# Performance work log

Hardware: AMD Instinct MI355X
Metric: run time of the kernel (lower is better)

Reference implementation:

```python
import math
import jax, jax.numpy as jnp
import numpy as np

NUM_EXPERTS = 8
TOP_K = 2
HIDDEN = 1024
INTER = 4096
CAPACITY_FACTOR = 1.25
S, B = 2048, 4


def setup_inputs() -> dict:
    key = jax.random.key(0)
    k1, k2, k3, k4 = jax.random.split(key, 4)
    hidden_states = jax.random.normal(k1, (S, B, HIDDEN), dtype=jnp.float32)
    T = S * B
    logits = jax.random.normal(k2, (T, NUM_EXPERTS), dtype=jnp.float32)
    expert_affinities = jax.nn.softmax(logits, axis=-1)  # (T, E), normalized per token
    # top-k chosen experts per token (no duplicates), consistent with affinities
    _, expert_index = jax.lax.top_k(expert_affinities, TOP_K)  # (T, top_k) int32
    gate_up_proj = jax.random.normal(k3, (NUM_EXPERTS, HIDDEN, 2 * INTER), dtype=jnp.float32) * 0.02
    down_proj = jax.random.normal(k4, (NUM_EXPERTS, INTER, HIDDEN), dtype=jnp.float32) * 0.02
    return {
        "hidden_states": hidden_states,
        "expert_affinities": expert_affinities,
        "expert_index": expert_index.astype(jnp.int32),
        "gate_up_proj": gate_up_proj,
        "down_proj": down_proj,
    }


def reference(hidden_states, expert_affinities, expert_index, gate_up_proj, down_proj):
    S_, B_, H = hidden_states.shape
    T = S_ * B_
    E = expert_affinities.shape[1]
    K = expert_index.shape[1]
    # expert capacity (static, as in compute_position_in_expert)
    C = min(math.ceil(T * K * CAPACITY_FACTOR / E), T)

    x = hidden_states.reshape(T, H)

    # top_k-hot expert mask (T, E)
    expert_mask = jnp.sum(jax.nn.one_hot(expert_index, E, dtype=jnp.int32), axis=1)
    # 1-indexed position of each token within each chosen expert
    position_in_expert = jnp.cumsum(expert_mask, axis=0) * expert_mask  # (T, E)
    kept = (expert_mask > 0) & (position_in_expert <= C)  # capacity drop
    pos0 = position_in_expert - 1  # 0-indexed

    # gather per-(token, k) positions / keep flags
    pos_tk = jnp.take_along_axis(pos0, expert_index, axis=1)          # (T, K)
    kept_tk = jnp.take_along_axis(kept, expert_index, axis=1)         # (T, K)
    flat_idx = jnp.where(kept_tk, expert_index * C + pos_tk, E * C)   # dropped -> dummy slot

    # dispatch: scatter tokens into per-expert buffers (E*C [+1 dummy], H)
    src = jnp.broadcast_to(x[:, None, :], (T, K, H)).reshape(T * K, H)
    dispatched = jnp.zeros((E * C + 1, H), dtype=x.dtype).at[flat_idx.reshape(-1)].add(src)
    expert_buf = dispatched[: E * C].reshape(E, C, H)

    # grouped expert MLP (GLU): gate/up projection, SiLU gating, down projection
    gate_up = jnp.einsum("ech,ehf->ecf", expert_buf, gate_up_proj)    # (E, C, 2I)
    gate, up = jnp.split(gate_up, 2, axis=2)
    intermediate = jax.nn.silu(gate) * up                              # (E, C, I)
    expert_out = jnp.einsum("eci,eih->ech", intermediate, down_proj)   # (E, C, H)

    # combine: gather each token's expert outputs, weight by (normalized) affinities
    out_flat = jnp.concatenate(
        [expert_out.reshape(E * C, H), jnp.zeros((1, H), dtype=expert_out.dtype)], axis=0
    )
    aff_tk = jnp.take_along_axis(expert_affinities, expert_index, axis=1)  # (T, K)
    aff_tk = aff_tk / jnp.sum(aff_tk, axis=-1, keepdims=True)  # normalize_top_k_affinities
    weights = aff_tk * kept_tk.astype(aff_tk.dtype)            # dropped tokens contribute 0
    tok_out = jnp.sum(out_flat[flat_idx] * weights[..., None], axis=1)  # (T, H)
    return tok_out.reshape(S_, B_, H)
```

## Files before the change

kernel.cpp:

```cpp
#include <hip/hip_runtime.h>
#include <hip/hip_bf16.h>

#define NE 8
#define HID 1024
#define INT_ 4096
#define NTOK 8192
#define CAP 2560

typedef short short8 __attribute__((ext_vector_type(8)));
typedef float floatx4 __attribute__((ext_vector_type(4)));

__device__ __forceinline__ unsigned short f2bf(float f) {
  union { float f; unsigned int u; } v; v.f = f;
  unsigned int u = v.u;
  return (unsigned short)((u + 0x7fffu + ((u >> 16) & 1u)) >> 16);
}

__device__ __forceinline__ void gl2lds16(const void* g, void* l) {
  __builtin_amdgcn_global_load_lds(
      (const __attribute__((address_space(1))) unsigned int*)g,
      (__attribute__((address_space(3))) unsigned int*)l, 16, 0, 0);
}

__global__ void routing_kernel(const int* __restrict__ eidx,
                               int* __restrict__ tfs,
                               int* __restrict__ counts, int* __restrict__ slots) {
  __shared__ unsigned long long masks[128];
  __shared__ int ccnt[128];
  int e = blockIdx.x;
  int tid = threadIdx.x;
  int wave = tid >> 6, lane = tid & 63;

  for (int ch = wave; ch < 128; ch += 4) {
    int t = ch * 64 + lane;
    int2 pr = ((const int2*)eidx)[t];
    bool chosen = (pr.x == e) || (pr.y == e);
    unsigned long long m = __ballot(chosen);
    if (lane == 0) { masks[ch] = m; ccnt[ch] = __popcll(m); }
  }
  __syncthreads();
  if (tid == 0) {
    int run = 0;
    for (int i = 0; i < 128; ++i) { int c = ccnt[i]; ccnt[i] = run; run += c; }
    counts[e] = run < CAP ? run : CAP;
  }
  __syncthreads();
  for (int ch = wave; ch < 128; ch += 4) {
    int t = ch * 64 + lane;
    unsigned long long m = masks[ch];
    if ((m >> lane) & 1ull) {
      int pos = ccnt[ch] + __popcll(m & ((2ull << lane) - 1ull));
      int2 pr = ((const int2*)eidx)[t];
      int kk = (pr.x == e) ? 0 : 1;
      if (pos <= CAP) {
        int slot = e * CAP + pos - 1;
        tfs[slot] = t;
        slots[2 * t + kk] = slot;
      } else {
        slots[2 * t + kk] = -1;
      }
    }
  }
}

__global__ void transpose_cvt_kernel(const float* __restrict__ in, unsigned short* __restrict__ out,
                                     int R, int Cc) {
  __shared__ unsigned short tile[64 * 66];
  int z = blockIdx.z;
  int r0 = blockIdx.y * 64, c0 = blockIdx.x * 64;
  const float* inp = in + (size_t)z * R * Cc;
  unsigned short* outp = out + (size_t)z * R * Cc;
  int tx = threadIdx.x & 15, ty = threadIdx.x >> 4;
#pragma unroll
  for (int j = 0; j < 4; ++j) {
    int r = ty + j * 16;
    float4 v = *(const float4*)(inp + (size_t)(r0 + r) * Cc + c0 + 4 * tx);
    tile[r * 66 + 4 * tx + 0] = f2bf(v.x);
    tile[r * 66 + 4 * tx + 1] = f2bf(v.y);
    tile[r * 66 + 4 * tx + 2] = f2bf(v.z);
    tile[r * 66 + 4 * tx + 3] = f2bf(v.w);
  }
  __syncthreads();
#pragma unroll
  for (int j = 0; j < 4; ++j) {
    int c = ty + j * 16;
    ushort4 p;
    p.x = tile[(4 * tx + 0) * 66 + c];
    p.y = tile[(4 * tx + 1) * 66 + c];
    p.z = tile[(4 * tx + 2) * 66 + c];
    p.w = tile[(4 * tx + 3) * 66 + c];
    *(ushort4*)(outp + (size_t)(c0 + c) * R + r0 + 4 * tx) = p;
  }
}

__global__ void dispatch_kernel(const float* __restrict__ x, const int* __restrict__ tfs,
                                const int* __restrict__ counts, unsigned short* __restrict__ ebuf) {
  int slot = blockIdx.x;
  int e = slot / CAP, c = slot - e * CAP;
  bool valid = c < counts[e];
  int t = valid ? tfs[slot] : 0;
  const float4* src = (const float4*)(x + (size_t)t * HID);
  ushort4* dst = (ushort4*)(ebuf + (size_t)slot * HID);
#pragma unroll
  for (int j = 0; j < 2; ++j) {
    int i = threadIdx.x + j * 128;
    ushort4 p;
    if (valid) {
      float4 v = src[i];
      p.x = f2bf(v.x); p.y = f2bf(v.y); p.z = f2bf(v.z); p.w = f2bf(v.w);
    } else {
      p.x = p.y = p.z = p.w = 0;
    }
    dst[i] = p;
  }
}

__global__ void gemm1_kernel(const unsigned short* __restrict__ ebuf,
                             const unsigned short* __restrict__ wgu,
                             const int* __restrict__ counts,
                             unsigned short* __restrict__ inter) {
  int e = blockIdx.z;
  int c0 = blockIdx.y * 128;
  int f0 = blockIdx.x * 64;
  int cnt = counts[e];
  if (c0 >= cnt) return;

  __shared__ alignas(16) unsigned short smem[16384];
  unsigned short* sA = smem;
  unsigned short* sBg = smem + 8192;
  unsigned short* sBu = smem + 12288;

  int tid = threadIdx.x;
  int wave = tid >> 6, lane = tid & 63;
  int wm = (wave & 1) * 64;
  int isUp = wave >> 1;
  int lrow = lane >> 3, lch = lane & 7;
  int quad = lane >> 4, rl = lane & 15;

  const unsigned short* Ab = ebuf + ((size_t)e * CAP + c0) * HID;
  const unsigned short* Bb = wgu + ((size_t)e * 2 * INT_ + isUp * INT_ + f0) * HID;
  unsigned short* sB = isUp ? sBu : sBg;

  floatx4 acc[4][4];
#pragma unroll
  for (int i = 0; i < 4; ++i)
#pragma unroll
    for (int j = 0; j < 4; ++j) acc[i][j] = (floatx4){0.f, 0.f, 0.f, 0.f};

  for (int kk = 0; kk < HID; kk += 64) {
    __syncthreads();
#pragma unroll
    for (int i = 0; i < 4; ++i) {
      int r = wave * 32 + i * 8 + lrow;
      int gk = kk + ((lch ^ (r & 7)) << 3);
      gl2lds16(Ab + (size_t)r * HID + gk, sA + (wave * 32 + i * 8) * 64);
    }
#pragma unroll
    for (int i = 0; i < 4; ++i) {
      int r = (wave & 1) * 32 + i * 8 + lrow;
      int gk = kk + ((lch ^ (r & 7)) << 3);
      gl2lds16(Bb + (size_t)r * HID + gk, sB + ((wave & 1) * 32 + i * 8) * 64);
    }
    __syncthreads();
#pragma unroll
    for (int ks = 0; ks < 2; ++ks) {
      short8 a[4], b[4];
#pragma unroll
      for (int mi = 0; mi < 4; ++mi) {
        int r = wm + mi * 16 + rl;
        int pc = (ks * 4 + quad) ^ (r & 7);
        a[mi] = *(const short8*)(sA + r * 64 + pc * 8);
      }
#pragma unroll
      for (int ni = 0; ni < 4; ++ni) {
        int r = ni * 16 + rl;
        int pc = (ks * 4 + quad) ^ (r & 7);
        b[ni] = *(const short8*)(sB + r * 64 + pc * 8);
      }
#pragma unroll
      for (int mi = 0; mi < 4; ++mi)
#pragma unroll
        for (int ni = 0; ni < 4; ++ni)
          acc[mi][ni] = __builtin_amdgcn_mfma_f32_16x16x32_bf16(a[mi], b[ni], acc[mi][ni], 0, 0, 0);
    }
  }

  __syncthreads();
  float* gsh = (float*)smem;
  if (!isUp) {
#pragma unroll
    for (int mi = 0; mi < 4; ++mi)
#pragma unroll
      for (int ni = 0; ni < 4; ++ni)
#pragma unroll
        for (int r = 0; r < 4; ++r) {
          int row = wm + mi * 16 + quad * 4 + r;
          int col = ni * 16 + rl;
          gsh[row * 64 + col] = acc[mi][ni][r];
        }
  }
  __syncthreads();
  if (isUp) {
#pragma unroll
    for (int mi = 0; mi < 4; ++mi) {
#pragma unroll
      for (int r = 0; r < 4; ++r) {
        int row = wm + mi * 16 + quad * 4 + r;
#pragma unroll
        for (int ni = 0; ni < 4; ++ni) {
          int col = ni * 16 + rl;
          float g = gsh[row * 64 + col];
          float u = acc[mi][ni][r];
          float s = g / (1.f + __expf(-g));
          inter[((size_t)e * CAP + c0 + row) * INT_ + f0 + col] = f2bf(s * u);
        }
      }
    }
  }
}

__global__ void gemm2_kernel(const unsigned short* __restrict__ inter,
                             const unsigned short* __restrict__ wd,
                             const int* __restrict__ counts,
                             float* __restrict__ eout) {
  int e = blockIdx.z;
  int c0 = blockIdx.y * 128;
  int h0 = blockIdx.x * 128;
  int cnt = counts[e];
  if (c0 >= cnt) return;

  __shared__ alignas(16) unsigned short smem[16384];
  unsigned short* sA = smem;
  unsigned short* sB = smem + 8192;

  int tid = threadIdx.x;
  int wave = tid >> 6, lane = tid & 63;
  int wm = (wave & 1) * 64, wn = (wave >> 1) * 64;
  int lrow = lane >> 3, lch = lane & 7;
  int quad = lane >> 4, rl = lane & 15;

  const unsigned short* Ab = inter + ((size_t)e * CAP + c0) * INT_;
  const unsigned short* Bb = wd + ((size_t)e * HID + h0) * INT_;

  floatx4 acc[4][4];
#pragma unroll
  for (int i = 0; i < 4; ++i)
#pragma unroll
    for (int j = 0; j < 4; ++j) acc[i][j] = (floatx4){0.f, 0.f, 0.f, 0.f};

  for (int kk = 0; kk < INT_; kk += 64) {
    __syncthreads();
#pragma unroll
    for (int i = 0; i < 4; ++i) {
      int r = wave * 32 + i * 8 + lrow;
      int gk = kk + ((lch ^ (r & 7)) << 3);
      gl2lds16(Ab + (size_t)r * INT_ + gk, sA + (wave * 32 + i * 8) * 64);
      gl2lds16(Bb + (size_t)r * INT_ + gk, sB + (wave * 32 + i * 8) * 64);
    }
    __syncthreads();
#pragma unroll
    for (int ks = 0; ks < 2; ++ks) {
      short8 a[4], b[4];
#pragma unroll
      for (int mi = 0; mi < 4; ++mi) {
        int r = wm + mi * 16 + rl;
        int pc = (ks * 4 + quad) ^ (r & 7);
        a[mi] = *(const short8*)(sA + r * 64 + pc * 8);
      }
#pragma unroll
      for (int ni = 0; ni < 4; ++ni) {
        int r = wn + ni * 16 + rl;
        int pc = (ks * 4 + quad) ^ (r & 7);
        b[ni] = *(const short8*)(sB + r * 64 + pc * 8);
      }
#pragma unroll
      for (int mi = 0; mi < 4; ++mi)
#pragma unroll
        for (int ni = 0; ni < 4; ++ni)
          acc[mi][ni] = __builtin_amdgcn_mfma_f32_16x16x32_bf16(a[mi], b[ni], acc[mi][ni], 0, 0, 0);
    }
  }

#pragma unroll
  for (int mi = 0; mi < 4; ++mi) {
#pragma unroll
    for (int r = 0; r < 4; ++r) {
      int row = wm + mi * 16 + quad * 4 + r;
      float* op = eout + ((size_t)e * CAP + c0 + row) * HID + h0;
#pragma unroll
      for (int ni = 0; ni < 4; ++ni) op[wn + ni * 16 + rl] = acc[mi][ni][r];
    }
  }
}

__global__ void combine_kernel(const float4* __restrict__ eout, const int* __restrict__ slots,
                               const float* __restrict__ aff, const int* __restrict__ eidx,
                               float4* __restrict__ out) {
  int t = blockIdx.x;
  int i = threadIdx.x;
  int s0 = slots[2 * t], s1 = slots[2 * t + 1];
  int e0 = eidx[2 * t], e1 = eidx[2 * t + 1];
  float a0 = aff[t * NE + e0], a1 = aff[t * NE + e1];
  float inv = 1.f / (a0 + a1);
  float w0 = (s0 >= 0) ? a0 * inv : 0.f;
  float w1 = (s1 >= 0) ? a1 * inv : 0.f;
  int p0 = (s0 >= 0) ? s0 : 0;
  int p1 = (s1 >= 0) ? s1 : 0;
  float4 v0 = eout[(size_t)p0 * 256 + i];
  float4 v1 = eout[(size_t)p1 * 256 + i];
  float4 r;
  r.x = w0 * v0.x + w1 * v1.x;
  r.y = w0 * v0.y + w1 * v1.y;
  r.z = w0 * v0.z + w1 * v1.z;
  r.w = w0 * v0.w + w1 * v1.w;
  out[(size_t)t * 256 + i] = r;
}

extern "C" void kernel_launch(void* const* d_in, const int* in_sizes, int n_in,
                              void* d_out, int out_size, void* d_ws, size_t ws_size,
                              hipStream_t stream) {
  const float* x = (const float*)d_in[0];
  const float* aff = (const float*)d_in[1];
  const int* eidx = (const int*)d_in[2];
  const float* wgu_f = (const float*)d_in[3];
  const float* wd_f = (const float*)d_in[4];
  float* out = (float*)d_out;

  char* ws = (char*)d_ws;
  int* tfs = (int*)(ws + 0);
  int* counts = (int*)(ws + 163840);
  int* slots = (int*)(ws + 196608);
  unsigned short* ebuf = (unsigned short*)(ws + 262144);
  unsigned short* wgu = (unsigned short*)(ws + 42205184);
  unsigned short* wd = (unsigned short*)(ws + 176422912);
  unsigned short* inter = (unsigned short*)(ws + 243531776);
  float* eout = (float*)(ws + 42205184);

  routing_kernel<<<NE, 256, 0, stream>>>(eidx, tfs, counts, slots);
  transpose_cvt_kernel<<<dim3(128, 16, NE), 256, 0, stream>>>(wgu_f, wgu, 1024, 8192);
  transpose_cvt_kernel<<<dim3(16, 64, NE), 256, 0, stream>>>(wd_f, wd, 4096, 1024);
  dispatch_kernel<<<NE * CAP, 128, 0, stream>>>(x, tfs, counts, ebuf);
  gemm1_kernel<<<dim3(64, 20, NE), 256, 0, stream>>>(ebuf, wgu, counts, inter);
  gemm2_kernel<<<dim3(8, 20, NE), 256, 0, stream>>>(inter, wd, counts, eout);
  combine_kernel<<<NTOK, 256, 0, stream>>>((const float4*)eout, slots, aff, eidx, (float4*)out);
}
```

Baseline: 1.054 ms.

## Replace both expert GEMMs with 256x256 double-buffered pipelined MFMA kernel

Replaces the separate 128x64 and 128x128 GEMM kernels with one templated 256x256-tile kernel (512 threads, 8 waves). It double-buffers LDS with global_load_lds, interleaves staging with quarter-tile MFMA phases using explicit vmcnt waits, raw barriers and setprio. The GLU variant keeps gate and up accumulators in the same wave, so the SiLU product is formed in registers without an LDS exchange. The goal is more data reuse per tile and hiding load latency behind MFMAs. The cost is 128KB of LDS and heavy register use, and the larger tiles may waste more work on partially filled expert capacity blocks.

```diff
diff --git a/kernel.cpp b/kernel.cpp
--- a/kernel.cpp
+++ b/kernel.cpp
@@ -115,180 +115,160 @@
   }
 }
 
-__global__ void gemm1_kernel(const unsigned short* __restrict__ ebuf,
-                             const unsigned short* __restrict__ wgu,
-                             const int* __restrict__ counts,
-                             unsigned short* __restrict__ inter) {
+
+#define BARX() do { asm volatile("" ::: "memory"); __builtin_amdgcn_s_barrier(); \
+  __builtin_amdgcn_sched_barrier(0); asm volatile("" ::: "memory"); } while (0)
+#define VMW4() asm volatile("s_waitcnt vmcnt(4)" ::: "memory")
+
+#define STAGE_A(SBUF, HALF, KT) do { \
+  _Pragma("unroll") for (int rr = 0; rr < 2; ++rr) { \
+    int lrow_ = (HALF) * 128 + rr * 64 + (tid >> 3); \
+    int gk_ = (KT) + (((tid & 7) ^ (lrow_ & 7)) << 3); \
+    gl2lds16(Ab + (size_t)lrow_ * KD + gk_, \
+             (SBUF) + ((HALF) * 128 + rr * 64 + wave * 8) * 64); \
+  } } while (0)
+
+#define STAGE_B(SBUF, HALF, KT) do { \
+  _Pragma("unroll") for (int rr = 0; rr < 2; ++rr) { \
+    int sr_ = rr * 64 + (tid >> 3); \
+    int gk_ = (KT) + (((tid & 7) ^ (sr_ & 7)) << 3); \
+    gl2lds16(((HALF) ? Bb1 : Bb0) + (size_t)sr_ * KD + gk_, \
+             (SBUF) + 16384 + ((HALF) * 128 + rr * 64 + wave * 8) * 64); \
+  } } while (0)
+
+#define LDA_Q(SBUF, QM) do { \
+  _Pragma("unroll") for (int ml = 0; ml < 4; ++ml) { \
+    int rA_ = (QM) * 128 + w_m * 64 + ml * 16 + rl; \
+    _Pragma("unroll") for (int ks = 0; ks < 2; ++ks) { \
+      int pc_ = (ks * 4 + quad) ^ (rA_ & 7); \
+      a[ml][ks] = *(const short8*)((SBUF) + rA_ * 64 + pc_ * 8); \
+    } } } while (0)
+
+#define LDB_Q(SBUF, QN, BREG) do { \
+  _Pragma("unroll") for (int nl = 0; nl < 2; ++nl) { \
+    int rB_ = (QN) * 128 + w_n * 32 + nl * 16 + rl; \
+    _Pragma("unroll") for (int ks = 0; ks < 2; ++ks) { \
+      int pc_ = (ks * 4 + quad) ^ (rB_ & 7); \
+      BREG[nl][ks] = *(const short8*)((SBUF) + 16384 + rB_ * 64 + pc_ * 8); \
+    } } } while (0)
+
+#define MFMA_Q(QM, QN, BREG) do { \
+  __builtin_amdgcn_s_setprio(1); \
+  _Pragma("unroll") for (int ml = 0; ml < 4; ++ml) \
+    _Pragma("unroll") for (int nl = 0; nl < 2; ++nl) \
+      _Pragma("unroll") for (int ks = 0; ks < 2; ++ks) \
+        acc[(QM) * 4 + ml][(QN) * 2 + nl] = __builtin_amdgcn_mfma_f32_16x16x32_bf16( \
+            a[ml][ks], BREG[nl][ks], acc[(QM) * 4 + ml][(QN) * 2 + nl], 0, 0, 0); \
+  __builtin_amdgcn_s_setprio(0); \
+} while (0)
+
+template <int KD, bool GLU>
+__global__ __launch_bounds__(512, 2) void gemm256_kernel(
+    const unsigned short* __restrict__ A, const unsigned short* __restrict__ B,
+    const int* __restrict__ counts, unsigned short* __restrict__ obf,
+    float* __restrict__ of) {
   int e = blockIdx.z;
-  int c0 = blockIdx.y * 128;
-  int f0 = blockIdx.x * 64;
-  int cnt = counts[e];
-  if (c0 >= cnt) return;
-
-  __shared__ alignas(16) unsigned short smem[16384];
-  unsigned short* sA = smem;
-  unsigned short* sBg = smem + 8192;
-  unsigned short* sBu = smem + 12288;
+  int c0 = blockIdx.y * 256;
+  if (c0 >= counts[e]) return;
+
+  __shared__ alignas(16) unsigned short smem[65536];
+  unsigned short* s0 = smem;
+  unsigned short* s1 = smem + 32768;
 
   int tid = threadIdx.x;
   int wave = tid >> 6, lane = tid & 63;
-  int wm = (wave & 1) * 64;
-  int isUp = wave >> 1;
-  int lrow = lane >> 3, lch = lane & 7;
-  int quad = lane >> 4, rl = lane & 15;
-
-  const unsigned short* Ab = ebuf + ((size_t)e * CAP + c0) * HID;
-  const unsigned short* Bb = wgu + ((size_t)e * 2 * INT_ + isUp * INT_ + f0) * HID;
-  unsigned short* sB = isUp ? sBu : sBg;
-
-  floatx4 acc[4][4];
-#pragma unroll
-  for (int i = 0; i < 4; ++i)
+  int w_m = wave >> 2, w_n = wave & 3;
+  int rl = lane & 15, quad = lane >> 4;
+
+  const unsigned short* Ab = A + ((size_t)e * CAP + c0) * KD;
+  const unsigned short* Bb0;
+  const unsigned short* Bb1;
+  int n0;
+  if constexpr (GLU) {
+    n0 = blockIdx.x * 128;
+    Bb0 = B + ((size_t)e * 2 * INT_ + n0) * KD;
+    Bb1 = B + ((size_t)e * 2 * INT_ + INT_ + n0) * KD;
+  } else {
+    n0 = blockIdx.x * 256;
+    Bb0 = B + ((size_t)e * HID + n0) * KD;
+    Bb1 = Bb0 + (size_t)128 * KD;
+  }
+
+  short8 a[4][2], b0[2][2], b1[2][2];
+  floatx4 acc[8][4];
+#pragma unroll
+  for (int i = 0; i < 8; ++i)
 #pragma unroll
     for (int j = 0; j < 4; ++j) acc[i][j] = (floatx4){0.f, 0.f, 0.f, 0.f};
 
-  for (int kk = 0; kk < HID; kk += 64) {
-    __syncthreads();
-#pragma unroll
-    for (int i = 0; i < 4; ++i) {
-      int r = wave * 32 + i * 8 + lrow;
-      int gk = kk + ((lch ^ (r & 7)) << 3);
-      gl2lds16(Ab + (size_t)r * HID + gk, sA + (wave * 32 + i * 8) * 64);
-    }
-#pragma unroll
-    for (int i = 0; i < 4; ++i) {
-      int r = (wave & 1) * 32 + i * 8 + lrow;
-      int gk = kk + ((lch ^ (r & 7)) << 3);
-      gl2lds16(Bb + (size_t)r * HID + gk, sB + ((wave & 1) * 32 + i * 8) * 64);
-    }
-    __syncthreads();
-#pragma unroll
-    for (int ks = 0; ks < 2; ++ks) {
-      short8 a[4], b[4];
-#pragma unroll
-      for (int mi = 0; mi < 4; ++mi) {
-        int r = wm + mi * 16 + rl;
-        int pc = (ks * 4 + quad) ^ (r & 7);
-        a[mi] = *(const short8*)(sA + r * 64 + pc * 8);
-      }
-#pragma unroll
-      for (int ni = 0; ni < 4; ++ni) {
-        int r = ni * 16 + rl;
-        int pc = (ks * 4 + quad) ^ (r & 7);
-        b[ni] = *(const short8*)(sB + r * 64 + pc * 8);
-      }
-#pragma unroll
-      for (int mi = 0; mi < 4; ++mi)
-#pragma unroll
-        for (int ni = 0; ni < 4; ++ni)
-          acc[mi][ni] = __builtin_amdgcn_mfma_f32_16x16x32_bf16(a[mi], b[ni], acc[mi][ni], 0, 0, 0);
-    }
-  }
-
-  __syncthreads();
-  float* gsh = (float*)smem;
-  if (!isUp) {
-#pragma unroll
-    for (int mi = 0; mi < 4; ++mi)
-#pragma unroll
-      for (int ni = 0; ni < 4; ++ni)
+  STAGE_A(s0, 0, 0);
+  STAGE_B(s0, 0, 0);
+  STAGE_B(s0, 1, 0);
+  STAGE_A(s0, 1, 0);
+  VMW4();
+  BARX();
+
+  for (int it = 0; it < KD / 128; ++it) {
+    int kt1 = it * 128 + 64;
+    int ktn = (it * 128 + 128 < KD) ? (it * 128 + 128) : 0;
+    LDA_Q(s0, 0);
+    LDB_Q(s0, 0, b0);
+    STAGE_A(s1, 0, kt1);
+    VMW4(); BARX();
+    MFMA_Q(0, 0, b0);
+    LDB_Q(s0, 1, b1);
+    STAGE_B(s1, 0, kt1);
+    VMW4(); BARX();
+    MFMA_Q(0, 1, b1);
+    LDA_Q(s0, 1);
+    STAGE_B(s1, 1, kt1);
+    BARX();
+    MFMA_Q(1, 1, b1);
+    STAGE_A(s1, 1, kt1);
+    VMW4(); BARX();
+    MFMA_Q(1, 0, b0);
+    LDA_Q(s1, 0);
+    LDB_Q(s1, 0, b0);
+    STAGE_A(s0, 0, ktn);
+    VMW4(); BARX();
+    MFMA_Q(0, 0, b0);
+    LDB_Q(s1, 1, b1);
+    STAGE_B(s0, 0, ktn);
+    VMW4(); BARX();
+    MFMA_Q(0, 1, b1);
+    LDA_Q(s1, 1);
+    STAGE_B(s0, 1, ktn);
+    BARX();
+    MFMA_Q(1, 1, b1);
+    STAGE_A(s0, 1, ktn);
+    VMW4(); BARX();
+    MFMA_Q(1, 0, b0);
+  }
+  asm volatile("s_waitcnt vmcnt(0)" ::: "memory");
+
+#pragma unroll
+  for (int mi = 0; mi < 8; ++mi) {
+    int row = (mi >> 2) * 128 + w_m * 64 + (mi & 3) * 16 + quad * 4;
+    if constexpr (GLU) {
+#pragma unroll
+      for (int nl = 0; nl < 2; ++nl) {
+        int col = n0 + w_n * 32 + nl * 16 + rl;
 #pragma unroll
         for (int r = 0; r < 4; ++r) {
-          int row = wm + mi * 16 + quad * 4 + r;
-          int col = ni * 16 + rl;
-          gsh[row * 64 + col] = acc[mi][ni][r];
-        }
-  }
-  __syncthreads();
-  if (isUp) {
-#pragma unroll
-    for (int mi = 0; mi < 4; ++mi) {
-#pragma unroll
-      for (int r = 0; r < 4; ++r) {
-        int row = wm + mi * 16 + quad * 4 + r;
-#pragma unroll
-        for (int ni = 0; ni < 4; ++ni) {
-          int col = ni * 16 + rl;
-          float g = gsh[row * 64 + col];
-          float u = acc[mi][ni][r];
+          float g = acc[mi][nl][r];
+          float u = acc[mi][nl + 2][r];
           float s = g / (1.f + __expf(-g));
-          inter[((size_t)e * CAP + c0 + row) * INT_ + f0 + col] = f2bf(s * u);
+          obf[((size_t)e * CAP + c0 + row + r) * INT_ + col] = f2bf(s * u);
         }
       }
-    }
-  }
-}
-
-__global__ void gemm2_kernel(const unsigned short* __restrict__ inter,
-                             const unsigned short* __restrict__ wd,
-                             const int* __restrict__ counts,
-                             float* __restrict__ eout) {
-  int e = blockIdx.z;
-  int c0 = blockIdx.y * 128;
-  int h0 = blockIdx.x * 128;
-  int cnt = counts[e];
-  if (c0 >= cnt) return;
-
-  __shared__ alignas(16) unsigned short smem[16384];
-  unsigned short* sA = smem;
-  unsigned short* sB = smem + 8192;
-
-  int tid = threadIdx.x;
-  int wave = tid >> 6, lane = tid & 63;
-  int wm = (wave & 1) * 64, wn = (wave >> 1) * 64;
-  int lrow = lane >> 3, lch = lane & 7;
-  int quad = lane >> 4, rl = lane & 15;
-
-  const unsigned short* Ab = inter + ((size_t)e * CAP + c0) * INT_;
-  const unsigned short* Bb = wd + ((size_t)e * HID + h0) * INT_;
-
-  floatx4 acc[4][4];
-#pragma unroll
-  for (int i = 0; i < 4; ++i)
-#pragma unroll
-    for (int j = 0; j < 4; ++j) acc[i][j] = (floatx4){0.f, 0.f, 0.f, 0.f};
-
-  for (int kk = 0; kk < INT_; kk += 64) {
-    __syncthreads();
-#pragma unroll
-    for (int i = 0; i < 4; ++i) {
-      int r = wave * 32 + i * 8 + lrow;
-      int gk = kk + ((lch ^ (r & 7)) << 3);
-      gl2lds16(Ab + (size_t)r * INT_ + gk, sA + (wave * 32 + i * 8) * 64);
-      gl2lds16(Bb + (size_t)r * INT_ + gk, sB + (wave * 32 + i * 8) * 64);
-    }
-    __syncthreads();
-#pragma unroll
-    for (int ks = 0; ks < 2; ++ks) {
-      short8 a[4], b[4];
-#pragma unroll
-      for (int mi = 0; mi < 4; ++mi) {
-        int r = wm + mi * 16 + rl;
-        int pc = (ks * 4 + quad) ^ (r & 7);
-        a[mi] = *(const short8*)(sA + r * 64 + pc * 8);
+    } else {
+#pragma unroll
+      for (int ni = 0; ni < 4; ++ni) {
+        int col = n0 + (ni >> 1) * 128 + w_n * 32 + (ni & 1) * 16 + rl;
+#pragma unroll
+        for (int r = 0; r < 4; ++r)
+          of[((size_t)e * CAP + c0 + row + r) * HID + col] = acc[mi][ni][r];
       }
-#pragma unroll
-      for (int ni = 0; ni < 4; ++ni) {
-        int r = wn + ni * 16 + rl;
-        int pc = (ks * 4 + quad) ^ (r & 7);
-        b[ni] = *(const short8*)(sB + r * 64 + pc * 8);
-      }
-#pragma unroll
-      for (int mi = 0; mi < 4; ++mi)
-#pragma unroll
-        for (int ni = 0; ni < 4; ++ni)
-          acc[mi][ni] = __builtin_amdgcn_mfma_f32_16x16x32_bf16(a[mi], b[ni], acc[mi][ni], 0, 0, 0);
-    }
-  }
-
-#pragma unroll
-  for (int mi = 0; mi < 4; ++mi) {
-#pragma unroll
-    for (int r = 0; r < 4; ++r) {
-      int row = wm + mi * 16 + quad * 4 + r;
-      float* op = eout + ((size_t)e * CAP + c0 + row) * HID + h0;
-#pragma unroll
-      for (int ni = 0; ni < 4; ++ni) op[wn + ni * 16 + rl] = acc[mi][ni][r];
     }
   }
 }
@@ -340,7 +320,9 @@
   transpose_cvt_kernel<<<dim3(128, 16, NE), 256, 0, stream>>>(wgu_f, wgu, 1024, 8192);
   transpose_cvt_kernel<<<dim3(16, 64, NE), 256, 0, stream>>>(wd_f, wd, 4096, 1024);
   dispatch_kernel<<<NE * CAP, 128, 0, stream>>>(x, tfs, counts, ebuf);
-  gemm1_kernel<<<dim3(64, 20, NE), 256, 0, stream>>>(ebuf, wgu, counts, inter);
-  gemm2_kernel<<<dim3(8, 20, NE), 256, 0, stream>>>(inter, wd, counts, eout);
+  gemm256_kernel<HID, true><<<dim3(32, 10, NE), 512, 0, stream>>>(
+      ebuf, wgu, counts, inter, (float*)nullptr);
+  gemm256_kernel<INT_, false><<<dim3(4, 10, NE), 512, 0, stream>>>(
+      inter, wd, counts, (unsigned short*)nullptr, eout);
   combine_kernel<<<NTOK, 256, 0, stream>>>((const float4*)eout, slots, aff, eidx, (float4*)out);
 }
```

Measured after the change: 998.2 us. 1.06x faster.
